# Optimization experiments

Measured on AMD Instinct MI355X. Metric: run time of the kernel, lower is better.

The kernel has to match this reference:

```python
import jax, jax.numpy as jnp
import numpy as np

B, H, W, N = 4, 64, 64, 64
NEAR, FAR = 2.0, 6.0
HID = 64


def setup_inputs() -> dict:
    key = jax.random.key(0)
    ks = jax.random.split(key, 6)
    ray_origins = jnp.tile(jnp.array([0.0, 0.0, 4.0], jnp.float32), (B, H, W, 1))
    ray_directions = jax.random.normal(ks[0], (B, H, W, 3), jnp.float32)
    tform_cam2world = jnp.eye(4, dtype=jnp.float32) + 0.1 * jax.random.normal(ks[1], (B, 4, 4), jnp.float32)
    depth_noise = jax.random.uniform(ks[2], (B, H, W, N), jnp.float32)
    u_samples = jax.random.uniform(ks[3], (B, H, W, N), jnp.float32)
    W1 = 0.5 * jax.random.normal(ks[4], (3, HID), jnp.float32)
    b1 = jnp.zeros((HID,), jnp.float32)
    W2 = 0.5 * jax.random.normal(ks[5], (HID, 4), jnp.float32)
    b2 = jnp.zeros((4,), jnp.float32)
    return dict(ray_origins=ray_origins, ray_directions=ray_directions,
                tform_cam2world=tform_cam2world, depth_noise=depth_noise,
                u_samples=u_samples, W1=W1, b1=b1, W2=W2, b2=b2)


def field(pts, W1, b1, W2, b2):
    # tiny radiance-field MLP standing in for the generator's sampler
    h = jax.nn.relu(pts @ W1 + b1)
    out = h @ W2 + b2
    sigma = out[..., 0]
    rgb = jax.nn.sigmoid(out[..., 1:4])
    return sigma, rgb


def compositing_weights(sigma, z_vals):
    # alpha-compositing weights (render_volume_density)
    dists = jnp.concatenate([z_vals[..., 1:] - z_vals[..., :-1],
                             jnp.full_like(z_vals[..., :1], 1e10)], axis=-1)
    alpha = 1.0 - jnp.exp(-jax.nn.relu(sigma) * dists)
    trans = jnp.cumprod(1.0 - alpha + 1e-10, axis=-1)
    trans = jnp.concatenate([jnp.ones_like(trans[..., :1]), trans[..., :-1]], axis=-1)
    return alpha * trans


def sample_pdf(bins, weights, u):
    # bins [R, M+1], weights [R, M], u [R, S] -> samples [R, S]
    pdf = weights / jnp.sum(weights, axis=-1, keepdims=True)
    cdf = jnp.cumsum(pdf, axis=-1)
    cdf = jnp.concatenate([jnp.zeros_like(cdf[..., :1]), cdf], axis=-1)  # [R, M+1]
    inds = jax.vmap(lambda c, uu: jnp.searchsorted(c, uu, side='right'))(cdf, u)
    last = cdf.shape[-1] - 1
    below = jnp.clip(inds - 1, 0, last)
    above = jnp.clip(inds, 0, last)
    cdf_b = jnp.take_along_axis(cdf, below, axis=-1)
    cdf_a = jnp.take_along_axis(cdf, above, axis=-1)
    bin_b = jnp.take_along_axis(bins, below, axis=-1)
    bin_a = jnp.take_along_axis(bins, above, axis=-1)
    denom = cdf_a - cdf_b
    denom = jnp.where(denom < 1e-5, 1.0, denom)
    t = (u - cdf_b) / denom
    return bin_b + t * (bin_a - bin_b)


def reference(ray_origins, ray_directions, tform_cam2world, depth_noise, u_samples, W1, b1, W2, b2):
    rd = ray_directions / jnp.linalg.norm(ray_directions, axis=-1, keepdims=True)
    # stratified coarse samples along each ray
    t = (jnp.arange(N, dtype=jnp.float32) + depth_noise) / N           # [B,H,W,N]
    z_vals = NEAR + (FAR - NEAR) * t
    pts = ray_origins[..., None, :] + rd[..., None, :] * z_vals[..., None]
    sigma, rgb = field(pts, W1, b1, W2, b2)                            # [B,H,W,N], [B,H,W,N,3]

    # --- hierarchical importance sampling (no_grad in original) ---
    w = compositing_weights(sigma, z_vals).reshape(-1, N)              # [R,N]
    pad = jnp.pad(w, ((0, 0), (1, 1)), constant_values=-jnp.inf)
    mx = jnp.maximum(pad[:, :-1], pad[:, 1:])                          # max_pool1d(k=2,s=1,p=1) -> [R,N+1]
    sm = 0.5 * (mx[:, :-1] + mx[:, 1:]) + 0.01                        # avg_pool1d(k=2,s=1)  -> [R,N]
    z_mid = (0.5 * (z_vals[..., 1:] + z_vals[..., :-1])).reshape(-1, N - 1)
    z_samples = sample_pdf(z_mid, sm[:, 1:-1], u_samples.reshape(-1, N))
    z_samples = jax.lax.stop_gradient(z_samples.reshape(B, H, W, N))

    # fine evaluation + merge-sort of coarse/fine samples
    z_all = jnp.concatenate([z_vals, z_samples], axis=-1)              # [B,H,W,2N]
    idx = jnp.argsort(z_all, axis=-1)
    z_sorted = jnp.take_along_axis(z_all, idx, axis=-1)
    pts_f = ray_origins[..., None, :] + rd[..., None, :] * z_samples[..., None]
    sigma_f, rgb_f = field(pts_f, W1, b1, W2, b2)
    sigma_all = jnp.take_along_axis(jnp.concatenate([sigma, sigma_f], axis=-1), idx, axis=-1)
    rgb_cat = jnp.concatenate([rgb, rgb_f], axis=-2)
    rgb_all = jnp.take_along_axis(rgb_cat, jnp.broadcast_to(idx[..., None], idx.shape + (3,)), axis=-2)

    # final alpha compositing
    w_all = compositing_weights(sigma_all, z_sorted)
    rgb_pred = jnp.sum(w_all[..., None] * rgb_all, axis=-2)            # [B,H,W,3]
    depth_pred = jnp.sum(w_all * z_sorted, axis=-1)                    # [B,H,W]
    mask_pred = jnp.sum(w_all, axis=-1)                                # [B,H,W]

    # camera-space depth (invert_space: R_w2c = R^T)
    R_w2c = jnp.swapaxes(tform_cam2world[:, :3, :3], -1, -2)           # [B,3,3]
    view_dir = jnp.einsum('bhwj,bij->bhwi', rd, R_w2c)
    depth_cam = -(view_dir * depth_pred[..., None])[..., -1]
    return rgb_pred, depth_cam, mask_pred
```

## Files before the change

kernel.cpp:

```cpp
#include <hip/hip_runtime.h>
#include <hip/hip_bf16.h>
#include <math.h>

#define Nn    64
#define RPB   4
#define NRAYS 16384
#define NEARV 2.0f
#define FARV  6.0f

typedef __attribute__((ext_vector_type(8))) short bf16x8;
typedef __attribute__((ext_vector_type(4))) float f32x4;
typedef __attribute__((ext_vector_type(2))) float f32x2;

template <int CTRL, int RMASK>
__device__ __forceinline__ float dpp_mv(float x, float ident) {
  return __int_as_float(__builtin_amdgcn_update_dpp(
      __float_as_int(ident), __float_as_int(x), CTRL, RMASK, 0xf, false));
}
__device__ __forceinline__ float scan_add_dpp(float x) {
  x += dpp_mv<0x111, 0xf>(x, 0.f);
  x += dpp_mv<0x112, 0xf>(x, 0.f);
  x += dpp_mv<0x114, 0xf>(x, 0.f);
  x += dpp_mv<0x118, 0xf>(x, 0.f);
  x += dpp_mv<0x142, 0xa>(x, 0.f);
  x += dpp_mv<0x143, 0xc>(x, 0.f);
  return x;
}
__device__ __forceinline__ float scan_mul_dpp(float x) {
  x *= dpp_mv<0x111, 0xf>(x, 1.f);
  x *= dpp_mv<0x112, 0xf>(x, 1.f);
  x *= dpp_mv<0x114, 0xf>(x, 1.f);
  x *= dpp_mv<0x118, 0xf>(x, 1.f);
  x *= dpp_mv<0x142, 0xa>(x, 1.f);
  x *= dpp_mv<0x143, 0xc>(x, 1.f);
  return x;
}
__device__ __forceinline__ float reduce_add_bcast(float x) {
  x = scan_add_dpp(x);
  return __int_as_float(__builtin_amdgcn_readlane(__float_as_int(x), 63));
}

__device__ __forceinline__ float fast_rcp(float x) { return __builtin_amdgcn_rcpf(x); }
__device__ __forceinline__ float sigmoidf_fast(float x) { return fast_rcp(1.f + __expf(-x)); }

__device__ __forceinline__ short bfhi_bits(float x) { return (short)(__float_as_uint(x) >> 16); }
__device__ __forceinline__ float bfhi_val(float x)  { return __uint_as_float(__float_as_uint(x) & 0xFFFF0000u); }

__device__ __forceinline__ int count_le_reg(float arr, float x, int bound) {
  int cnt = 0;
#pragma unroll
  for (int step = 64; step >= 1; step >>= 1) {
    const int idx = cnt + step - 1;
    const float v = __shfl(arr, idx, 64);
    if (idx < bound && v <= x) cnt += step;
  }
  return cnt;
}
__device__ __forceinline__ int count_lt_reg(float arr, float x, int bound) {
  int cnt = 0;
#pragma unroll
  for (int step = 64; step >= 1; step >>= 1) {
    const int idx = cnt + step - 1;
    const float v = __shfl(arr, idx, 64);
    if (idx < bound && v < x) cnt += step;
  }
  return cnt;
}

__device__ __forceinline__ void field_eval(
    float zlane, const f32x2 c0v[2][4], const f32x2 c1v[2][4],
    const bf16x8 aHi[2], const bf16x8 aLo[2],
    float b20, float b21, float b22, float b23,
    int quad, int col, float4* scratch, float o[4]) {
  const bool q0 = (quad == 0);
#pragma unroll
  for (int nt = 0; nt < 4; ++nt) {
    f32x4 acc;
    acc[0] = q0 ? b20 : 0.f;
    acc[1] = q0 ? b21 : 0.f;
    acc[2] = q0 ? b22 : 0.f;
    acc[3] = q0 ? b23 : 0.f;
    const float zm = __shfl(zlane, nt * 16 + col, 64);
    const f32x2 zm2 = {zm, zm};
#pragma unroll
    for (int ks = 0; ks < 2; ++ks) {
      union { bf16x8 v; unsigned u[4]; } Bhi, Blo;
#pragma unroll
      for (int p = 0; p < 4; ++p) {
        f32x2 h = zm2 * c1v[ks][p] + c0v[ks][p];
        h = __builtin_elementwise_max(h, (f32x2){0.f, 0.f});
        union { f32x2 f; unsigned u[2]; } U; U.f = h;
        Bhi.u[p] = __builtin_amdgcn_perm(U.u[1], U.u[0], 0x07060302u);
        union { unsigned u[2]; f32x2 f; } M;
        M.u[0] = U.u[0] & 0xFFFF0000u;
        M.u[1] = U.u[1] & 0xFFFF0000u;
        const f32x2 l = h - M.f;
        union { f32x2 f; unsigned u[2]; } L; L.f = l;
        Blo.u[p] = __builtin_amdgcn_perm(L.u[1], L.u[0], 0x07060302u);
      }
      acc = __builtin_amdgcn_mfma_f32_16x16x32_bf16(aHi[ks], Bhi.v, acc, 0, 0, 0);
      acc = __builtin_amdgcn_mfma_f32_16x16x32_bf16(aHi[ks], Blo.v, acc, 0, 0, 0);
      acc = __builtin_amdgcn_mfma_f32_16x16x32_bf16(aLo[ks], Bhi.v, acc, 0, 0, 0);
    }
    if (quad == 0) scratch[nt * 16 + col] = make_float4(acc[0], acc[1], acc[2], acc[3]);
  }
  const float4 r = scratch[(threadIdx.x & 63)];
  o[0] = r.x; o[1] = r.y; o[2] = r.z; o[3] = r.w;
}

__global__ __launch_bounds__(RPB * 64, 4) void nerf_fused(
    const float* __restrict__ ray_o, const float* __restrict__ ray_d,
    const float* __restrict__ tform, const float* __restrict__ noise,
    const float* __restrict__ usmp,  const float* __restrict__ W1,
    const float* __restrict__ b1,    const float* __restrict__ W2,
    const float* __restrict__ b2,    float* __restrict__ out) {
  const int wave = threadIdx.x >> 6;
  const int lane = threadIdx.x & 63;
  const int ray  = blockIdx.x * RPB + wave;
  const int quad = lane >> 4;
  const int col  = lane & 15;

  __shared__ float2 sC [RPB][Nn];
  __shared__ float  sZs[RPB][2 * Nn];
  __shared__ float4 sPk[RPB][2 * Nn];

  const float o0 = ray_o[ray * 3 + 0], o1 = ray_o[ray * 3 + 1], o2 = ray_o[ray * 3 + 2];
  float d0 = ray_d[ray * 3 + 0], d1 = ray_d[ray * 3 + 1], d2 = ray_d[ray * 3 + 2];
  const float rn = __builtin_amdgcn_rsqf(d0 * d0 + d1 * d1 + d2 * d2);
  d0 *= rn; d1 *= rn; d2 *= rn;

  {
    const float w10 = W1[lane], w11 = W1[64 + lane], w12 = W1[128 + lane];
    const float c1 = d0 * w10 + d1 * w11 + d2 * w12;
    const float c0 = o0 * w10 + o1 * w11 + o2 * w12 + b1[lane];
    sC[wave][lane] = make_float2(c0, c1);
  }

  const float nz = noise[ray * Nn + lane];
  const float z  = NEARV + (FARV - NEARV) * ((float)lane + nz) * (1.0f / Nn);

  f32x2 c0v[2][4], c1v[2][4];
#pragma unroll
  for (int ks = 0; ks < 2; ++ks) {
    const float4* cc4 = (const float4*)&sC[wave][0];
    const int base4 = (ks * 32 + quad * 8) >> 1;
#pragma unroll
    for (int jj = 0; jj < 4; ++jj) {
      const float4 v = cc4[base4 + jj];
      c0v[ks][jj] = (f32x2){v.x, v.z};
      c1v[ks][jj] = (f32x2){v.y, v.w};
    }
  }

  bf16x8 aHi[2], aLo[2];
#pragma unroll
  for (int ks = 0; ks < 2; ++ks) {
#pragma unroll
    for (int j = 0; j < 8; ++j) {
      const int k = ks * 32 + quad * 8 + j;
      const float wv  = (col < 4) ? W2[k * 4 + col] : 0.f;
      aHi[ks][j] = bfhi_bits(wv);
      aLo[ks][j] = bfhi_bits(wv - bfhi_val(wv));
    }
  }
  const float b20 = b2[0], b21 = b2[1], b22 = b2[2], b23 = b2[3];
  float4* scratch = &sPk[wave][0];

  float oc[4];
  field_eval(z, c0v, c1v, aHi, aLo, b20, b21, b22, b23, quad, col, scratch, oc);
  const float sig = oc[0];
  const float cr = sigmoidf_fast(oc[1]), cg = sigmoidf_fast(oc[2]), cb = sigmoidf_fast(oc[3]);

  const float zn   = __shfl_down(z, 1, 64);
  const float dist = (lane == 63) ? 1e10f : (zn - z);
  const float alpha = 1.f - __expf(-fmaxf(sig, 0.f) * dist);
  float cdfreg, binreg;
  {
    const float P  = scan_mul_dpp(1.f - alpha + 1e-10f);
    float Te = __shfl_up(P, 1, 64);
    if (lane == 0) Te = 1.f;
    const float w = alpha * Te;

    const float wp = __shfl_up(w, 1, 64);
    const float wn = __shfl_down(w, 1, 64);
    const float mxA = (lane == 0)  ? w : fmaxf(wp, w);
    const float mxB = (lane == 63) ? w : fmaxf(w, wn);
    const float sm = 0.5f * (mxA + mxB) + 0.01f;

    const float v   = (lane >= 1 && lane <= 62) ? sm : 0.f;
    const float tot = reduce_add_bcast(v);
    const float pdf = v * fast_rcp(tot);
    const float C   = scan_add_dpp(pdf);
    cdfreg = (lane == 0) ? 0.f : C;
    binreg = 0.5f * (z + zn);
  }

  const float u = usmp[ray * Nn + lane];
  const int lo = count_le_reg(cdfreg, u, 63);
  const int below = lo - 1;
  const int above = (lo < 63) ? lo : 62;
  const float cdfb = __shfl(cdfreg, below, 64);
  const float cdfa = __shfl(cdfreg, above, 64);
  const float binb = __shfl(binreg, below, 64);
  const float bina = __shfl(binreg, above, 64);
  float den = cdfa - cdfb;
  if (den < 1e-5f) den = 1.f;
  const float zs = fmaf((u - cdfb) * fast_rcp(den), bina - binb, binb);

  float of[4];
  field_eval(zs, c0v, c1v, aHi, aLo, b20, b21, b22, b23, quad, col, scratch, of);
  const float sigF = of[0];
  const float fr = sigmoidf_fast(of[1]), fg = sigmoidf_fast(of[2]), fb = sigmoidf_fast(of[3]);

  int r1 = 0;
#pragma unroll
  for (int j = 0; j < 64; ++j) {
    const float zj = __int_as_float(__builtin_amdgcn_readlane(__float_as_int(zs), j));
    r1 += (zj < zs) ? 1 : 0;
    r1 += (zj == zs && j < lane) ? 1 : 0;
  }
  const int lo1 = count_le_reg(z, zs, 64);
  const float zFs = __int_as_float(
      __builtin_amdgcn_ds_permute(r1 << 2, __float_as_int(zs)));
  const int lo2 = count_lt_reg(zFs, z, 64);
  const int p0 = lane + lo2;
  const int p1 = r1 + lo1;

  sZs[wave][p0] = z;
  sZs[wave][p1] = zs;
  sPk[wave][p0] = make_float4(sig,  cr, cg, cb);
  sPk[wave][p1] = make_float4(sigF, fr, fg, fb);

  const float2 zz = *(const float2*)&sZs[wave][2 * lane];
  const float z0 = zz.x, z1 = zz.y;
  const float z2 = __shfl_down(z0, 1, 64);
  const float dist0 = z1 - z0;
  const float dist1 = (lane == 63) ? 1e10f : (z2 - z1);
  const float4 q0 = sPk[wave][2 * lane];
  const float4 q1 = sPk[wave][2 * lane + 1];
  const float al0 = 1.f - __expf(-fmaxf(q0.x, 0.f) * dist0);
  const float al1 = 1.f - __expf(-fmaxf(q1.x, 0.f) * dist1);
  const float aa0 = 1.f - al0 + 1e-10f;
  const float aa1 = 1.f - al1 + 1e-10f;
  const float Pp = scan_mul_dpp(aa0 * aa1);
  float Tp = __shfl_up(Pp, 1, 64);
  if (lane == 0) Tp = 1.f;
  const float w0 = al0 * Tp;
  const float w1 = al1 * Tp * aa0;

  const float accR = reduce_add_bcast(w0 * q0.y + w1 * q1.y);
  const float accG = reduce_add_bcast(w0 * q0.z + w1 * q1.z);
  const float accB = reduce_add_bcast(w0 * q0.w + w1 * q1.w);
  const float accD = reduce_add_bcast(w0 * z0 + w1 * z1);
  const float accM = reduce_add_bcast(w0 + w1);

  if (lane == 0) {
    const float* tf = tform + (ray >> 12) * 16;
    const float vz = d0 * tf[2] + d1 * tf[6] + d2 * tf[10];
    out[ray * 3 + 0]     = accR;
    out[ray * 3 + 1]     = accG;
    out[ray * 3 + 2]     = accB;
    out[NRAYS * 3 + ray] = -vz * accD;
    out[NRAYS * 4 + ray] = accM;
  }
}

extern "C" void kernel_launch(void* const* d_in, const int* in_sizes, int n_in,
                              void* d_out, int out_size, void* d_ws, size_t ws_size,
                              hipStream_t stream) {
  const float* ray_o = (const float*)d_in[0];
  const float* ray_d = (const float*)d_in[1];
  const float* tform = (const float*)d_in[2];
  const float* noise = (const float*)d_in[3];
  const float* usmp  = (const float*)d_in[4];
  const float* W1    = (const float*)d_in[5];
  const float* b1    = (const float*)d_in[6];
  const float* W2    = (const float*)d_in[7];
  const float* b2    = (const float*)d_in[8];
  float* out = (float*)d_out;

  nerf_fused<<<dim3(NRAYS / RPB), RPB * 64, 0, stream>>>(
      ray_o, ray_d, tform, noise, usmp, W1, b1, W2, b2, out);
}
```

Measured before the change: 114.9 us.

## Rank fine samples with packed integer keys and swizzle/bpermute instead of readlane loop

Replaces the 64-iteration readlane rank loop with packed unsigned keys (float bits shifted, with the lane index as tiebreak) compared through ds_swizzle and ds_bpermute exchanges. The merge searches now use these integer keys. Neighbor shuffles become wave-wide DPP row shifts, and the output bias add moves after the MFMA. The key packing assumes z lies in [2,8) so the exponent offset and the shift stay in range. This works for the near/far bounds used here but would break outside them.

```diff
diff --git a/kernel.cpp b/kernel.cpp
--- a/kernel.cpp
+++ b/kernel.cpp
@@ -16,6 +16,14 @@
 __device__ __forceinline__ float dpp_mv(float x, float ident) {
   return __int_as_float(__builtin_amdgcn_update_dpp(
       __float_as_int(ident), __float_as_int(x), CTRL, RMASK, 0xf, false));
+}
+__device__ __forceinline__ float shfl_up1(float x) {
+  return __int_as_float(__builtin_amdgcn_update_dpp(
+      __float_as_int(x), __float_as_int(x), 0x138, 0xf, 0xf, false));
+}
+__device__ __forceinline__ float shfl_dn1(float x) {
+  return __int_as_float(__builtin_amdgcn_update_dpp(
+      __float_as_int(x), __float_as_int(x), 0x130, 0xf, 0xf, false));
 }
 __device__ __forceinline__ float scan_add_dpp(float x) {
   x += dpp_mv<0x111, 0xf>(x, 0.f);
@@ -46,23 +54,30 @@
 __device__ __forceinline__ short bfhi_bits(float x) { return (short)(__float_as_uint(x) >> 16); }
 __device__ __forceinline__ float bfhi_val(float x)  { return __uint_as_float(__float_as_uint(x) & 0xFFFF0000u); }
 
-__device__ __forceinline__ int count_le_reg(float arr, float x, int bound) {
+template <int T>
+__device__ __forceinline__ void rank_swz(unsigned kf, int& r) {
+  const unsigned o = (unsigned)__builtin_amdgcn_ds_swizzle((int)kf, (T << 10) | 0x1F);
+  r += (o < kf) ? 1 : 0;
+  if constexpr (T + 1 < 32) rank_swz<T + 1>(kf, r);
+}
+
+__device__ __forceinline__ int count_lt_key(unsigned arr, unsigned x) {
+  int cnt = 0;
+#pragma unroll
+  for (int step = 64; step >= 1; step >>= 1) {
+    const int idx = cnt + step - 1;
+    const unsigned v = (unsigned)__shfl((int)arr, idx, 64);
+    if (idx < 64 && v < x) cnt += step;
+  }
+  return cnt;
+}
+__device__ __forceinline__ int count_le_f(float arr, float x) {
   int cnt = 0;
 #pragma unroll
   for (int step = 64; step >= 1; step >>= 1) {
     const int idx = cnt + step - 1;
     const float v = __shfl(arr, idx, 64);
-    if (idx < bound && v <= x) cnt += step;
-  }
-  return cnt;
-}
-__device__ __forceinline__ int count_lt_reg(float arr, float x, int bound) {
-  int cnt = 0;
-#pragma unroll
-  for (int step = 64; step >= 1; step >>= 1) {
-    const int idx = cnt + step - 1;
-    const float v = __shfl(arr, idx, 64);
-    if (idx < bound && v < x) cnt += step;
+    if (idx < 63 && v <= x) cnt += step;
   }
   return cnt;
 }
@@ -72,14 +87,9 @@
     const bf16x8 aHi[2], const bf16x8 aLo[2],
     float b20, float b21, float b22, float b23,
     int quad, int col, float4* scratch, float o[4]) {
-  const bool q0 = (quad == 0);
 #pragma unroll
   for (int nt = 0; nt < 4; ++nt) {
-    f32x4 acc;
-    acc[0] = q0 ? b20 : 0.f;
-    acc[1] = q0 ? b21 : 0.f;
-    acc[2] = q0 ? b22 : 0.f;
-    acc[3] = q0 ? b23 : 0.f;
+    f32x4 acc = {0.f, 0.f, 0.f, 0.f};
     const float zm = __shfl(zlane, nt * 16 + col, 64);
     const f32x2 zm2 = {zm, zm};
 #pragma unroll
@@ -105,7 +115,7 @@
     if (quad == 0) scratch[nt * 16 + col] = make_float4(acc[0], acc[1], acc[2], acc[3]);
   }
   const float4 r = scratch[(threadIdx.x & 63)];
-  o[0] = r.x; o[1] = r.y; o[2] = r.z; o[3] = r.w;
+  o[0] = r.x + b20; o[1] = r.y + b21; o[2] = r.z + b22; o[3] = r.w + b23;
 }
 
 __global__ __launch_bounds__(RPB * 64, 4) void nerf_fused(
@@ -138,6 +148,7 @@
 
   const float nz = noise[ray * Nn + lane];
   const float z  = NEARV + (FARV - NEARV) * ((float)lane + nz) * (1.0f / Nn);
+  const unsigned kc = ((__float_as_uint(z) - 0x40000000u) << 7) | (unsigned)lane;
 
   f32x2 c0v[2][4], c1v[2][4];
 #pragma unroll
@@ -171,20 +182,18 @@
   const float sig = oc[0];
   const float cr = sigmoidf_fast(oc[1]), cg = sigmoidf_fast(oc[2]), cb = sigmoidf_fast(oc[3]);
 
-  const float zn   = __shfl_down(z, 1, 64);
+  const float zn   = shfl_dn1(z);
   const float dist = (lane == 63) ? 1e10f : (zn - z);
   const float alpha = 1.f - __expf(-fmaxf(sig, 0.f) * dist);
   float cdfreg, binreg;
   {
     const float P  = scan_mul_dpp(1.f - alpha + 1e-10f);
-    float Te = __shfl_up(P, 1, 64);
+    float Te = shfl_up1(P);
     if (lane == 0) Te = 1.f;
     const float w = alpha * Te;
 
-    const float wp = __shfl_up(w, 1, 64);
-    const float wn = __shfl_down(w, 1, 64);
-    const float mxA = (lane == 0)  ? w : fmaxf(wp, w);
-    const float mxB = (lane == 63) ? w : fmaxf(w, wn);
+    const float mxA = fmaxf(shfl_up1(w), w);
+    const float mxB = fmaxf(w, shfl_dn1(w));
     const float sm = 0.5f * (mxA + mxB) + 0.01f;
 
     const float v   = (lane >= 1 && lane <= 62) ? sm : 0.f;
@@ -196,7 +205,7 @@
   }
 
   const float u = usmp[ray * Nn + lane];
-  const int lo = count_le_reg(cdfreg, u, 63);
+  const int lo = count_le_f(cdfreg, u);
   const int below = lo - 1;
   const int above = (lo < 63) ? lo : 62;
   const float cdfb = __shfl(cdfreg, below, 64);
@@ -212,17 +221,20 @@
   const float sigF = of[0];
   const float fr = sigmoidf_fast(of[1]), fg = sigmoidf_fast(of[2]), fb = sigmoidf_fast(of[3]);
 
+  const unsigned kf = ((__float_as_uint(zs) - 0x40000000u) << 7) | (unsigned)(64 + lane);
+
   int r1 = 0;
-#pragma unroll
-  for (int j = 0; j < 64; ++j) {
-    const float zj = __int_as_float(__builtin_amdgcn_readlane(__float_as_int(zs), j));
-    r1 += (zj < zs) ? 1 : 0;
-    r1 += (zj == zs && j < lane) ? 1 : 0;
-  }
-  const int lo1 = count_le_reg(z, zs, 64);
-  const float zFs = __int_as_float(
-      __builtin_amdgcn_ds_permute(r1 << 2, __float_as_int(zs)));
-  const int lo2 = count_lt_reg(zFs, z, 64);
+  rank_swz<1>(kf, r1);
+  const int xaddr = (lane ^ 32) << 2;
+#pragma unroll
+  for (int s = 0; s < 32; ++s) {
+    const unsigned o = (unsigned)__builtin_amdgcn_ds_bpermute(xaddr ^ (s << 2), (int)kf);
+    r1 += (o < kf) ? 1 : 0;
+  }
+
+  const int lo1 = count_lt_key(kc, kf);
+  const unsigned kfS = (unsigned)__builtin_amdgcn_ds_permute(r1 << 2, (int)kf);
+  const int lo2 = count_lt_key(kfS, kc);
   const int p0 = lane + lo2;
   const int p1 = r1 + lo1;
 
@@ -233,7 +245,7 @@
 
   const float2 zz = *(const float2*)&sZs[wave][2 * lane];
   const float z0 = zz.x, z1 = zz.y;
-  const float z2 = __shfl_down(z0, 1, 64);
+  const float z2 = shfl_dn1(z0);
   const float dist0 = z1 - z0;
   const float dist1 = (lane == 63) ? 1e10f : (z2 - z1);
   const float4 q0 = sPk[wave][2 * lane];
@@ -243,7 +255,7 @@
   const float aa0 = 1.f - al0 + 1e-10f;
   const float aa1 = 1.f - al1 + 1e-10f;
   const float Pp = scan_mul_dpp(aa0 * aa1);
-  float Tp = __shfl_up(Pp, 1, 64);
+  float Tp = shfl_up1(Pp);
   if (lane == 0) Tp = 1.f;
   const float w0 = al0 * Tp;
   const float w1 = al1 * Tp * aa0;
```

Result: faster. 109.4 us (-4.8%).
